# Optimization experiments

Measured on AMD Instinct MI355X. Metric: run time of the kernel, lower is better.

Reference implementation:

```python
import jax, jax.numpy as jnp
import numpy as np

B, N, M, D = 2, 16384, 2048, 256
LN_EPS = 1e-5


def setup_inputs() -> dict:
    key = jax.random.key(0)
    ks = jax.random.split(key, 12)
    inv = 1.0 / np.sqrt(D)
    return {
        "p_xyz": jax.random.normal(ks[0], (B, N, 3), jnp.float32),
        "v_xyz": jax.random.normal(ks[1], (B, 3), jnp.float32),
        "p_features": jax.random.normal(ks[2], (B, N, D), jnp.float32),
        "v_features": jax.random.normal(ks[3], (B, M, D), jnp.float32),
        "Wq": jax.random.normal(ks[4], (D, D), jnp.float32) * inv,
        "bq": jnp.zeros((D,), jnp.float32),
        "Wk": jax.random.normal(ks[5], (D, D), jnp.float32) * inv,
        "bk": jnp.zeros((D,), jnp.float32),
        "Wv": jax.random.normal(ks[6], (D, D), jnp.float32) * inv,
        "bv": jnp.zeros((D,), jnp.float32),
        "Wp1": jax.random.normal(ks[7], (3, 3), jnp.float32) * (1.0 / np.sqrt(3.0)),
        "bp1": jnp.zeros((3,), jnp.float32),
        "ln_w": jnp.ones((3,), jnp.float32),
        "ln_b": jnp.zeros((3,), jnp.float32),
        "Wp2": jax.random.normal(ks[8], (3, D), jnp.float32) * (1.0 / np.sqrt(3.0)),
        "bp2": jnp.zeros((D,), jnp.float32),
    }


def reference(p_xyz, v_xyz, p_features, v_features,
              Wq, bq, Wk, bk, Wv, bv,
              Wp1, bp1, ln_w, ln_b, Wp2, bp2):
    d_model = Wq.shape[1]
    # dist: [B, N, 3] = |p_xyz - v_xyz| (v_xyz broadcast over N)
    dist = jnp.abs(p_xyz - v_xyz[:, None, :])
    # fc_p: Linear(3,3) -> LayerNorm(3) -> ReLU -> Linear(3, d_model)
    h = dist @ Wp1 + bp1                                   # [B, N, 3]
    mu = jnp.mean(h, axis=-1, keepdims=True)
    var = jnp.mean((h - mu) ** 2, axis=-1, keepdims=True)
    h = (h - mu) / jnp.sqrt(var + LN_EPS) * ln_w + ln_b
    pv = jax.nn.relu(h) @ Wp2 + bp2                        # [B, N, D]

    q = v_features @ Wq + bq                               # [B, M, D]
    k = p_features @ Wk + bk                               # [B, N, D]
    v = p_features @ Wv + bv                               # [B, N, D]

    # q@k^T + q@pv^T == q @ (k+pv)^T, scaled by sqrt(d_model)
    scale = 1.0 / jnp.sqrt(jnp.asarray(d_model, q.dtype))
    logits = jnp.einsum('bmd,bnd->bmn', q, k + pv) * scale  # [B, M, N]
    w = jax.nn.softmax(logits, axis=-2)                     # softmax over M (dim=-2)
    res = jnp.einsum('bmn,bnd->bmd', w, v)                  # [B, M, D]
    return res + v_features
```

## Files before the change

### kernel.cpp

```cpp
#include <hip/hip_runtime.h>
#include <math.h>

namespace {

constexpr int   B_ = 2;
constexpr int   N_ = 16384;
constexpr int   M_ = 2048;
constexpr int   D_ = 256;
constexpr float QS_ = 0.09016844005556021f;
constexpr float LN_EPS_ = 1e-5f;
constexpr int   NS_  = 16;
constexpr int   NPB_ = N_ / NS_;
constexpr int   NCOPY_ = 16;
constexpr int   NT16_ = N_ / 16;
constexpr int   MT32_ = M_ / 32;
constexpr size_t OUTSZ_ = (size_t)B_*M_*D_;

typedef _Float16 f16x8 __attribute__((ext_vector_type(8)));
typedef float    f32x16 __attribute__((ext_vector_type(16)));
typedef unsigned int u32x2 __attribute__((ext_vector_type(2)));

__device__ inline f16x8 as_h8(uint4 u) { return __builtin_bit_cast(f16x8, u); }
__device__ inline unsigned short f16bits(float x) {
    return __builtin_bit_cast(unsigned short, (_Float16)x);
}
__device__ inline unsigned int pack2(float a, float b) {
    return (unsigned int)f16bits(a) | ((unsigned int)f16bits(b) << 16);
}
__device__ inline uint4 pack8(const unsigned short v[8]) {
    return make_uint4((uint32_t)v[0] | ((uint32_t)v[1] << 16),
                      (uint32_t)v[2] | ((uint32_t)v[3] << 16),
                      (uint32_t)v[4] | ((uint32_t)v[5] << 16),
                      (uint32_t)v[6] | ((uint32_t)v[7] << 16));
}
#define MFMA16(acc, a, b) (acc) = __builtin_amdgcn_mfma_f32_32x32x16_f16((a), (b), (acc), 0, 0, 0)

__device__ inline int cd_row(int reg, int lane) {
    return (reg & 3) + 8 * (reg >> 2) + 4 * (lane >> 5);
}

__device__ inline size_t SP(int bloc, int g16, int tm) {
    return (((size_t)bloc * NT16_ + g16) * MT32_ + tm) * 64;
}

__global__ void prep_wt(const float* __restrict__ Wq, const float* __restrict__ Wk,
                        const float* __restrict__ Wv, uint4* __restrict__ wp) {
    __shared__ unsigned short ldb[256 * 33];
    const int mat = blockIdx.x >> 3;
    const int Tc  = blockIdx.x & 7;
    const float* W = (mat == 0) ? Wq : (mat == 1) ? Wk : Wv;
    const float scl = (mat == 0) ? QS_ : 1.0f;
    const int d = threadIdx.x;
    #pragma unroll
    for (int c = 0; c < 32; c += 4) {
        const float4 v = *reinterpret_cast<const float4*>(&W[d * D_ + Tc * 32 + c]);
        ldb[d * 33 + c + 0] = f16bits(v.x * scl);
        ldb[d * 33 + c + 1] = f16bits(v.y * scl);
        ldb[d * 33 + c + 2] = f16bits(v.z * scl);
        ldb[d * 33 + c + 3] = f16bits(v.w * scl);
    }
    __syncthreads();
    const int lane = threadIdx.x & 63;
    const int pg   = threadIdx.x >> 6;
    #pragma unroll
    for (int kq = 0; kq < 4; ++kq) {
        const int ks = pg * 4 + kq;
        unsigned short hh[8];
        #pragma unroll
        for (int j = 0; j < 8; ++j)
            hh[j] = ldb[(ks * 16 + (lane >> 5) * 8 + j) * 33 + (lane & 31)];
        wp[((size_t)((mat * 8 + Tc) * 16 + ks)) * 64 + lane] = pack8(hh);
    }
}

__global__ void prep_hr(const float* __restrict__ p_xyz, const float* __restrict__ v_xyz,
                        const float* __restrict__ Wp1, const float* __restrict__ bp1,
                        const float* __restrict__ ln_w, const float* __restrict__ ln_b,
                        float4* __restrict__ hr4) {
    const int r = blockIdx.x * 256 + threadIdx.x;
    if (r >= B_ * N_) return;
    const int b = r / N_;
    const float d0 = fabsf(p_xyz[r*3+0] - v_xyz[b*3+0]);
    const float d1 = fabsf(p_xyz[r*3+1] - v_xyz[b*3+1]);
    const float d2 = fabsf(p_xyz[r*3+2] - v_xyz[b*3+2]);
    float h[3];
    #pragma unroll
    for (int j = 0; j < 3; ++j)
        h[j] = d0*Wp1[0*3+j] + d1*Wp1[1*3+j] + d2*Wp1[2*3+j] + bp1[j];
    const float mu = (h[0]+h[1]+h[2]) * (1.0f/3.0f);
    const float e0 = h[0]-mu, e1 = h[1]-mu, e2 = h[2]-mu;
    const float var = (e0*e0 + e1*e1 + e2*e2) * (1.0f/3.0f);
    const float inv = rsqrtf(var + LN_EPS_);
    hr4[r] = make_float4(fmaxf(e0*inv*ln_w[0] + ln_b[0], 0.0f),
                         fmaxf(e1*inv*ln_w[1] + ln_b[1], 0.0f),
                         fmaxf(e2*inv*ln_w[2] + ln_b[2], 0.0f), 0.0f);
}

template<int MODE>
__global__ void gemm_qkv(const float* __restrict__ in,
                         const uint4* __restrict__ wp,
                         const float* __restrict__ bias,
                         const float4* __restrict__ hr4,
                         const float* __restrict__ Wp2, const float* __restrict__ bp2,
                         const float* __restrict__ sc, int roff32,
                         uint4* __restrict__ op) {
    __shared__ unsigned short tb[4][32 * 33];
    __shared__ float scb[64];
    const int tid  = threadIdx.x;
    const int lane = tid & 63;
    const int w    = tid >> 6;
    const int wr   = w & 1;
    const int wc   = w >> 1;
    const int lane31 = lane & 31;
    const int Trow = roff32 + blockIdx.x * 2 + wr;
    const int rowA = Trow * 32 + lane31;
    const float* ap = in + (size_t)rowA * D_ + (lane >> 5) * 8;

    if (MODE == 2) {
        if (tid < 64) scb[tid] = sc[(roff32 + blockIdx.x * 2) * 32 + tid];
        __syncthreads();
    }

    f32x16 acc[4];
    #pragma unroll
    for (int t = 0; t < 4; ++t) acc[t] = (f32x16)0.0f;

    union U8 { _Float16 f[8]; f16x8 v; };
    #pragma unroll 4
    for (int ks = 0; ks < 16; ++ks) {
        const float4 f0 = *reinterpret_cast<const float4*>(ap + ks*16);
        const float4 f1 = *reinterpret_cast<const float4*>(ap + ks*16 + 4);
        const float xs[8] = {f0.x, f0.y, f0.z, f0.w, f1.x, f1.y, f1.z, f1.w};
        U8 ah, al;
        #pragma unroll
        for (int j = 0; j < 8; ++j) {
            ah.f[j] = (_Float16)xs[j];
            al.f[j] = (_Float16)(xs[j] - (float)ah.f[j]);
        }
        #pragma unroll
        for (int t = 0; t < 4; ++t) {
            const f16x8 bh = as_h8(wp[((size_t)((wc * 4 + t) * 16 + ks)) * 64 + lane]);
            MFMA16(acc[t], ah.v, bh);
            MFMA16(acc[t], al.v, bh);
        }
    }

    const float bscale = (MODE == 0) ? QS_ : 1.0f;
    float biasc[4], w0c[4], w1c[4], w2c[4], b2c[4];
    #pragma unroll
    for (int t = 0; t < 4; ++t) {
        const int cc = wc * 128 + t * 32 + lane31;
        biasc[t] = bias[cc] * bscale;
        if (MODE == 1) {
            w0c[t] = Wp2[0*D_ + cc]; w1c[t] = Wp2[1*D_ + cc];
            w2c[t] = Wp2[2*D_ + cc]; b2c[t] = bp2[cc];
        }
    }
    float4 hv[16];
    if (MODE == 1) {
        #pragma unroll
        for (int r = 0; r < 16; ++r) hv[r] = hr4[Trow * 32 + cd_row(r, lane)];
    }

    #pragma unroll
    for (int t = 0; t < 4; ++t) {
        #pragma unroll
        for (int r = 0; r < 16; ++r) {
            float v = acc[t][r] + biasc[t];
            if (MODE == 1) v += hv[r].x*w0c[t] + hv[r].y*w1c[t] + hv[r].z*w2c[t] + b2c[t];
            if (MODE == 2) v *= scb[wr * 32 + cd_row(r, lane)];
            tb[w][cd_row(r, lane) * 33 + lane31] = f16bits(v);
        }
        if (MODE != 2) {
            #pragma unroll
            for (int p = 0; p < 2; ++p) {
                unsigned short hh[8];
                #pragma unroll
                for (int j = 0; j < 8; ++j)
                    hh[j] = tb[w][lane31 * 33 + p * 16 + (lane >> 5) * 8 + j];
                op[((size_t)(Trow * 16 + wc * 8 + t * 2 + p)) * 64 + lane] = pack8(hh);
            }
        } else {
            #pragma unroll
            for (int h16 = 0; h16 < 2; ++h16) {
                unsigned short hh[8];
                #pragma unroll
                for (int j = 0; j < 8; ++j)
                    hh[j] = tb[w][(h16 * 16 + (lane >> 5) * 8 + j) * 33 + lane31];
                op[((size_t)((Trow * 2 + h16) * 8 + wc * 4 + t)) * 64 + lane] = pack8(hh);
            }
        }
    }
}

template<int NB>
__global__ __launch_bounds__(256, 2)
void sgemm(const uint4* __restrict__ qp, const uint4* __restrict__ kp,
           uint4* __restrict__ sws, float* __restrict__ t0p, int b0) {
    const int tid  = threadIdx.x;
    const int lane = tid & 63;
    const int w    = tid >> 6;
    const int g    = blockIdx.x * 4 + w;
    const int mh   = g & 1;
    const int r    = g >> 1;
    const int bl   = (NB == 2) ? (r & 1) : 0;
    const int n32  = (NB == 2) ? (r >> 1) : r;
    const int b    = b0 + bl;
    const int Tn   = b * (N_ / 32) + n32;

    uint4 kf[16];
    #pragma unroll
    for (int ks = 0; ks < 16; ++ks)
        kf[ks] = kp[((size_t)(Tn * 16 + ks)) * 64 + lane];

    float tacc[16];
    #pragma unroll
    for (int q = 0; q < 16; ++q) tacc[q] = 0.0f;

    for (int t = 0; t < 32; ++t) {
        const int Tm = mh * 32 + t;
        uint4 qa[16];
        #pragma unroll
        for (int ks = 0; ks < 16; ++ks)
            qa[ks] = qp[((size_t)((b * MT32_ + Tm) * 16 + ks)) * 64 + lane];
        f32x16 sT0 = (f32x16)0.0f, sT1 = (f32x16)0.0f;
        #pragma unroll
        for (int ks = 0; ks < 16; ks += 2) {
            MFMA16(sT0, as_h8(kf[ks]),   as_h8(qa[ks]));
            MFMA16(sT1, as_h8(kf[ks+1]), as_h8(qa[ks+1]));
        }
        float ee[16];
        #pragma unroll
        for (int q = 0; q < 16; ++q) {
            ee[q] = exp2f(fminf(sT0[q] + sT1[q], 15.5f));
            tacc[q] += ee[q];
        }
        unsigned int pk[8];
        #pragma unroll
        for (int i = 0; i < 8; ++i) pk[i] = pack2(ee[2*i], ee[2*i+1]);
        const u32x2 r0 = __builtin_amdgcn_permlane32_swap(pk[0], pk[2], false, false);
        const u32x2 r1 = __builtin_amdgcn_permlane32_swap(pk[1], pk[3], false, false);
        const u32x2 r2 = __builtin_amdgcn_permlane32_swap(pk[4], pk[6], false, false);
        const u32x2 r3 = __builtin_amdgcn_permlane32_swap(pk[5], pk[7], false, false);
        sws[SP(bl, n32 * 2 + 0, Tm) + lane] = make_uint4(r0[0], r1[0], r0[1], r1[1]);
        sws[SP(bl, n32 * 2 + 1, Tm) + lane] = make_uint4(r2[0], r3[0], r2[1], r3[1]);
    }

    #pragma unroll
    for (int q = 0; q < 16; ++q) {
        #pragma unroll
        for (int off = 16; off; off >>= 1)
            tacc[q] += __shfl_xor(tacc[q], off, 64);
    }
    if ((lane & 31) == 0) {
        #pragma unroll
        for (int q = 0; q < 16; ++q) {
            const int n = n32 * 32 + cd_row(q, lane);
            t0p[((size_t)(mh * B_ + b)) * N_ + n] = tacc[q];
        }
    }
}

__global__ void calc_sc(const float* __restrict__ t0p, float* __restrict__ sc, int b0) {
    const int b   = b0 + (blockIdx.x >> 4);
    const int sl  = blockIdx.x & 15;
    const int tid = threadIdx.x;
    constexpr int CH = N_ / 4 / 16;
    const float4* p0 = (const float4*)(t0p + ((size_t)(0 * B_ + b)) * N_) + sl * CH;
    const float4* p1 = (const float4*)(t0p + ((size_t)(1 * B_ + b)) * N_) + sl * CH;
    float4* s4 = (float4*)(sc + (size_t)b * N_) + sl * CH;
    for (int i = tid; i < CH; i += 256) {
        const float4 a = p0[i], c = p1[i];
        float4 o;
        o.x = fminf(1.0f / (a.x + c.x), 60000.0f);
        o.y = fminf(1.0f / (a.y + c.y), 60000.0f);
        o.z = fminf(1.0f / (a.z + c.z), 60000.0f);
        o.w = fminf(1.0f / (a.w + c.w), 60000.0f);
        s4[i] = o;
    }
}

template<int NB>
__global__ __launch_bounds__(256, 3)
void attn_out(const uint4* __restrict__ sws, const uint4* __restrict__ vp,
              float* __restrict__ part, int b0) {
    const int tid  = threadIdx.x;
    const int lane = tid & 63;
    const int w    = tid >> 6;
    const int wm   = w & 1;
    const int wd   = w >> 1;
    const int lane31 = lane & 31;

    const int bid  = blockIdx.x;
    const int low3 = bid & 7;
    const int rest = bid >> 3;
    const int g    = (rest & (2*NB - 1)) * 8 + low3;
    const int bl   = g >> 4;
    const int b    = b0 + bl;
    const int ns   = g & 15;
    const int mt   = rest >> (NB == 2 ? 2 : 1);
    const int m0   = mt * 64;
    const int TmG  = mt * 2 + wm;

    f32x16 oacc[4];
    #pragma unroll
    for (int t = 0; t < 4; ++t) oacc[t] = (f32x16)0.0f;

    #pragma unroll 2
    for (int c = 0; c < NPB_ / 64; ++c) {
        const int nbase = ns * NPB_ + c * 64;
        const int g16   = nbase >> 4;
        uint4 af[4];
        #pragma unroll
        for (int t = 0; t < 4; ++t)
            af[t] = sws[SP(bl, g16 + t, TmG) + lane];
        const size_t gg0 = (size_t)((b * N_ + nbase) >> 4);
        #pragma unroll
        for (int k2 = 0; k2 < 4; ++k2) {
            #pragma unroll
            for (int dt = 0; dt < 4; ++dt) {
                MFMA16(oacc[dt], as_h8(af[k2]),
                       as_h8(vp[((gg0 + k2) * 8 + wd * 4 + dt) * 64 + lane]));
            }
        }
    }
    float* pb = part + (size_t)ns * OUTSZ_;
    #pragma unroll
    for (int dt = 0; dt < 4; ++dt) {
        #pragma unroll
        for (int r = 0; r < 16; ++r) {
            const int row = m0 + wm * 32 + cd_row(r, lane);
            pb[((size_t)(b * M_ + row)) * D_ + wd * 128 + dt * 32 + lane31] = oacc[dt][r];
        }
    }
}

__global__ void reduce_out(const float4* __restrict__ v, const float4* __restrict__ part,
                           float4* __restrict__ out) {
    const size_t i = (size_t)blockIdx.x * 256 + threadIdx.x;
    float4 a = v[i];
    #pragma unroll
    for (int c = 0; c < NCOPY_; ++c) {
        const float4 p = part[(size_t)c * (OUTSZ_ / 4) + i];
        a.x += p.x; a.y += p.y; a.z += p.z; a.w += p.w;
    }
    out[i] = a;
}

}

extern "C" void kernel_launch(void* const* d_in, const int* in_sizes, int n_in,
                              void* d_out, int out_size, void* d_ws, size_t ws_size,
                              hipStream_t stream) {
    const float* p_xyz      = (const float*)d_in[0];
    const float* v_xyz      = (const float*)d_in[1];
    const float* p_features = (const float*)d_in[2];
    const float* v_features = (const float*)d_in[3];
    const float* Wq  = (const float*)d_in[4];
    const float* bq  = (const float*)d_in[5];
    const float* Wk  = (const float*)d_in[6];
    const float* bk  = (const float*)d_in[7];
    const float* Wv  = (const float*)d_in[8];
    const float* bv  = (const float*)d_in[9];
    const float* Wp1 = (const float*)d_in[10];
    const float* bp1 = (const float*)d_in[11];
    const float* lnw = (const float*)d_in[12];
    const float* lnb = (const float*)d_in[13];
    const float* Wp2 = (const float*)d_in[14];
    const float* bp2 = (const float*)d_in[15];
    float* out = (float*)d_out;

    char* p = (char*)d_ws;
    auto alloc = [&](size_t bytes) {
        void* r = (void*)p;
        p += (bytes + 255) & ~(size_t)255;
        return r;
    };
    uint4* qpk = (uint4*)alloc((size_t)B_*M_*D_*2);
    uint4* kpk = (uint4*)alloc((size_t)B_*N_*D_*2);
    uint4* vpk = (uint4*)alloc((size_t)B_*N_*D_*2);
    uint4* wp  = (uint4*)alloc((size_t)3*D_*D_*2);
    float4* hr4 = (float4*)alloc((size_t)B_*N_*16);
    float*  t0p = (float*)alloc((size_t)2*B_*N_*4);
    float*  sc  = (float*)alloc((size_t)B_*N_*4);
    float*  part = (float*)alloc((size_t)NCOPY_*OUTSZ_*4);

    const size_t swsFull = (size_t)B_ * M_ * N_ * 2;
    const size_t used = (size_t)(p - (char*)d_ws);
    const bool full = ws_size >= used + swsFull;
    uint4* sws = (uint4*)alloc(full ? swsFull : swsFull / 2);

    constexpr size_t WMAT = (size_t)D_*D_/8;

    prep_wt<<<3*8, 256, 0, stream>>>(Wq, Wk, Wv, wp);
    prep_hr<<<(B_*N_)/256, 256, 0, stream>>>(p_xyz, v_xyz, Wp1, bp1, lnw, lnb, hr4);

    gemm_qkv<0><<<(B_*M_)/64, 256, 0, stream>>>(v_features, wp + 0*WMAT, bq, hr4, Wp2, bp2, nullptr, 0, qpk);
    gemm_qkv<1><<<(B_*N_)/64, 256, 0, stream>>>(p_features, wp + 1*WMAT, bk, hr4, Wp2, bp2, nullptr, 0, kpk);

    if (full) {
        sgemm<2><<<512, 256, 0, stream>>>(qpk, kpk, sws, t0p, 0);
        calc_sc<<<2*16, 256, 0, stream>>>(t0p, sc, 0);
        gemm_qkv<2><<<(B_*N_)/64, 256, 0, stream>>>(p_features, wp + 2*WMAT, bv, hr4, Wp2, bp2, sc, 0, vpk);
        attn_out<2><<<8*4*32, 256, 0, stream>>>(sws, vpk, part, 0);
    } else {
        for (int b = 0; b < B_; ++b) {
            sgemm<1><<<256, 256, 0, stream>>>(qpk, kpk, sws, t0p, b);
            calc_sc<<<16, 256, 0, stream>>>(t0p, sc, b);
            gemm_qkv<2><<<N_/64, 256, 0, stream>>>(p_features, wp + 2*WMAT, bv, hr4, Wp2, bp2, sc,
                                                   b * (N_/32), vpk);
            attn_out<1><<<8*2*32, 256, 0, stream>>>(sws, vpk, part, b);
        }
    }
    reduce_out<<<(OUTSZ_/4)/256, 256, 0, stream>>>((const float4*)v_features,
                                                   (const float4*)part, (float4*)out);
}
```

Before: 330.1 us.

## Split sgemm M range into quarters, prefetch Q tiles, nontemporal score stores

The score GEMM now splits each N tile's M range into four quarters instead of two, doubling the grid so more waves are in flight. The next Q tile is loaded right after the current MFMAs are issued, which overlaps global loads with the exp/pack work. Packing uses the hardware cvt_pkrtz instruction, and score tiles are written with nontemporal stores to avoid polluting cache. The column-sum partials grow to four per batch, so calc_sc reads four buffers and the partial-sum workspace doubles.

```diff
diff --git a/kernel.cpp b/kernel.cpp
--- a/kernel.cpp
+++ b/kernel.cpp
@@ -19,19 +19,22 @@
 typedef _Float16 f16x8 __attribute__((ext_vector_type(8)));
 typedef float    f32x16 __attribute__((ext_vector_type(16)));
 typedef unsigned int u32x2 __attribute__((ext_vector_type(2)));
+typedef unsigned int u32x4 __attribute__((ext_vector_type(4)));
 
 __device__ inline f16x8 as_h8(uint4 u) { return __builtin_bit_cast(f16x8, u); }
 __device__ inline unsigned short f16bits(float x) {
     return __builtin_bit_cast(unsigned short, (_Float16)x);
-}
-__device__ inline unsigned int pack2(float a, float b) {
-    return (unsigned int)f16bits(a) | ((unsigned int)f16bits(b) << 16);
 }
 __device__ inline uint4 pack8(const unsigned short v[8]) {
     return make_uint4((uint32_t)v[0] | ((uint32_t)v[1] << 16),
                       (uint32_t)v[2] | ((uint32_t)v[3] << 16),
                       (uint32_t)v[4] | ((uint32_t)v[5] << 16),
                       (uint32_t)v[6] | ((uint32_t)v[7] << 16));
+}
+__device__ inline void nt_store4(unsigned int a, unsigned int b,
+                                 unsigned int c, unsigned int d, uint4* dst) {
+    u32x4 v; v[0] = a; v[1] = b; v[2] = c; v[3] = d;
+    __builtin_nontemporal_store(v, reinterpret_cast<u32x4*>(dst));
 }
 #define MFMA16(acc, a, b) (acc) = __builtin_amdgcn_mfma_f32_32x32x16_f16((a), (b), (acc), 0, 0, 0)
 
@@ -201,8 +204,8 @@
     const int lane = tid & 63;
     const int w    = tid >> 6;
     const int g    = blockIdx.x * 4 + w;
-    const int mh   = g & 1;
-    const int r    = g >> 1;
+    const int mq   = g & 3;
+    const int r    = g >> 2;
     const int bl   = (NB == 2) ? (r & 1) : 0;
     const int n32  = (NB == 2) ? (r >> 1) : r;
     const int b    = b0 + bl;
@@ -217,33 +220,51 @@
     #pragma unroll
     for (int q = 0; q < 16; ++q) tacc[q] = 0.0f;
 
-    for (int t = 0; t < 32; ++t) {
-        const int Tm = mh * 32 + t;
-        uint4 qa[16];
-        #pragma unroll
-        for (int ks = 0; ks < 16; ++ks)
-            qa[ks] = qp[((size_t)((b * MT32_ + Tm) * 16 + ks)) * 64 + lane];
+    const size_t qstep = 16 * 64;
+    const size_t qb0 = ((size_t)((b * MT32_ + mq * 16) * 16)) * 64 + lane;
+
+    uint4 qa[16];
+    #pragma unroll
+    for (int ks = 0; ks < 16; ++ks) qa[ks] = qp[qb0 + (size_t)ks * 64];
+
+    for (int t = 0; t < 16; ++t) {
         f32x16 sT0 = (f32x16)0.0f, sT1 = (f32x16)0.0f;
         #pragma unroll
         for (int ks = 0; ks < 16; ks += 2) {
             MFMA16(sT0, as_h8(kf[ks]),   as_h8(qa[ks]));
             MFMA16(sT1, as_h8(kf[ks+1]), as_h8(qa[ks+1]));
         }
-        float ee[16];
-        #pragma unroll
-        for (int q = 0; q < 16; ++q) {
-            ee[q] = exp2f(fminf(sT0[q] + sT1[q], 15.5f));
-            tacc[q] += ee[q];
-        }
-        unsigned int pk[8];
-        #pragma unroll
-        for (int i = 0; i < 8; ++i) pk[i] = pack2(ee[2*i], ee[2*i+1]);
-        const u32x2 r0 = __builtin_amdgcn_permlane32_swap(pk[0], pk[2], false, false);
-        const u32x2 r1 = __builtin_amdgcn_permlane32_swap(pk[1], pk[3], false, false);
-        const u32x2 r2 = __builtin_amdgcn_permlane32_swap(pk[4], pk[6], false, false);
-        const u32x2 r3 = __builtin_amdgcn_permlane32_swap(pk[5], pk[7], false, false);
-        sws[SP(bl, n32 * 2 + 0, Tm) + lane] = make_uint4(r0[0], r1[0], r0[1], r1[1]);
-        sws[SP(bl, n32 * 2 + 1, Tm) + lane] = make_uint4(r2[0], r3[0], r2[1], r3[1]);
+        if (t < 15) {
+            const size_t qb = qb0 + (size_t)(t + 1) * qstep;
+            #pragma unroll
+            for (int ks = 0; ks < 16; ++ks) qa[ks] = qp[qb + (size_t)ks * 64];
+        }
+        const int Tm = mq * 16 + t;
+        unsigned int pk[4];
+        #pragma unroll
+        for (int i = 0; i < 4; ++i) {
+            const float e0 = exp2f(fminf(sT0[2*i]   + sT1[2*i],   15.5f));
+            const float e1 = exp2f(fminf(sT0[2*i+1] + sT1[2*i+1], 15.5f));
+            tacc[2*i] += e0; tacc[2*i+1] += e1;
+            pk[i] = __builtin_bit_cast(unsigned int, __builtin_amdgcn_cvt_pkrtz(e0, e1));
+        }
+        {
+            const u32x2 ra = __builtin_amdgcn_permlane32_swap(pk[0], pk[2], false, false);
+            const u32x2 rb = __builtin_amdgcn_permlane32_swap(pk[1], pk[3], false, false);
+            nt_store4(ra[0], rb[0], ra[1], rb[1], &sws[SP(bl, n32 * 2 + 0, Tm) + lane]);
+        }
+        #pragma unroll
+        for (int i = 0; i < 4; ++i) {
+            const float e0 = exp2f(fminf(sT0[2*i+8] + sT1[2*i+8], 15.5f));
+            const float e1 = exp2f(fminf(sT0[2*i+9] + sT1[2*i+9], 15.5f));
+            tacc[2*i+8] += e0; tacc[2*i+9] += e1;
+            pk[i] = __builtin_bit_cast(unsigned int, __builtin_amdgcn_cvt_pkrtz(e0, e1));
+        }
+        {
+            const u32x2 ra = __builtin_amdgcn_permlane32_swap(pk[0], pk[2], false, false);
+            const u32x2 rb = __builtin_amdgcn_permlane32_swap(pk[1], pk[3], false, false);
+            nt_store4(ra[0], rb[0], ra[1], rb[1], &sws[SP(bl, n32 * 2 + 1, Tm) + lane]);
+        }
     }
 
     #pragma unroll
@@ -256,7 +277,7 @@
         #pragma unroll
         for (int q = 0; q < 16; ++q) {
             const int n = n32 * 32 + cd_row(q, lane);
-            t0p[((size_t)(mh * B_ + b)) * N_ + n] = tacc[q];
+            t0p[((size_t)(mq * B_ + b)) * N_ + n] = tacc[q];
         }
     }
 }
@@ -268,14 +289,16 @@
     constexpr int CH = N_ / 4 / 16;
     const float4* p0 = (const float4*)(t0p + ((size_t)(0 * B_ + b)) * N_) + sl * CH;
     const float4* p1 = (const float4*)(t0p + ((size_t)(1 * B_ + b)) * N_) + sl * CH;
+    const float4* p2 = (const float4*)(t0p + ((size_t)(2 * B_ + b)) * N_) + sl * CH;
+    const float4* p3 = (const float4*)(t0p + ((size_t)(3 * B_ + b)) * N_) + sl * CH;
     float4* s4 = (float4*)(sc + (size_t)b * N_) + sl * CH;
     for (int i = tid; i < CH; i += 256) {
-        const float4 a = p0[i], c = p1[i];
+        const float4 a = p0[i], c = p1[i], d = p2[i], e = p3[i];
         float4 o;
-        o.x = fminf(1.0f / (a.x + c.x), 60000.0f);
-        o.y = fminf(1.0f / (a.y + c.y), 60000.0f);
-        o.z = fminf(1.0f / (a.z + c.z), 60000.0f);
-        o.w = fminf(1.0f / (a.w + c.w), 60000.0f);
+        o.x = fminf(1.0f / (a.x + c.x + d.x + e.x), 60000.0f);
+        o.y = fminf(1.0f / (a.y + c.y + d.y + e.y), 60000.0f);
+        o.z = fminf(1.0f / (a.z + c.z + d.z + e.z), 60000.0f);
+        o.w = fminf(1.0f / (a.w + c.w + d.w + e.w), 60000.0f);
         s4[i] = o;
     }
 }
@@ -381,7 +404,7 @@
     uint4* vpk = (uint4*)alloc((size_t)B_*N_*D_*2);
     uint4* wp  = (uint4*)alloc((size_t)3*D_*D_*2);
     float4* hr4 = (float4*)alloc((size_t)B_*N_*16);
-    float*  t0p = (float*)alloc((size_t)2*B_*N_*4);
+    float*  t0p = (float*)alloc((size_t)4*B_*N_*4);
     float*  sc  = (float*)alloc((size_t)B_*N_*4);
     float*  part = (float*)alloc((size_t)NCOPY_*OUTSZ_*4);
 
@@ -399,13 +422,13 @@
     gemm_qkv<1><<<(B_*N_)/64, 256, 0, stream>>>(p_features, wp + 1*WMAT, bk, hr4, Wp2, bp2, nullptr, 0, kpk);
 
     if (full) {
-        sgemm<2><<<512, 256, 0, stream>>>(qpk, kpk, sws, t0p, 0);
+        sgemm<2><<<1024, 256, 0, stream>>>(qpk, kpk, sws, t0p, 0);
         calc_sc<<<2*16, 256, 0, stream>>>(t0p, sc, 0);
         gemm_qkv<2><<<(B_*N_)/64, 256, 0, stream>>>(p_features, wp + 2*WMAT, bv, hr4, Wp2, bp2, sc, 0, vpk);
         attn_out<2><<<8*4*32, 256, 0, stream>>>(sws, vpk, part, 0);
     } else {
         for (int b = 0; b < B_; ++b) {
-            sgemm<1><<<256, 256, 0, stream>>>(qpk, kpk, sws, t0p, b);
+            sgemm<1><<<512, 256, 0, stream>>>(qpk, kpk, sws, t0p, b);
             calc_sc<<<16, 256, 0, stream>>>(t0p, sc, b);
             gemm_qkv<2><<<N_/64, 256, 0, stream>>>(p_features, wp + 2*WMAT, bv, hr4, Wp2, bp2, sc,
                                                    b * (N_/32), vpk);
```

Result: faster. 322.7 us (-2.2%).
